# Optimization experiments

Measured on AMD Instinct MI355X. Metric: run time of the kernel, lower is better.

## Reference

```python
import jax, jax.numpy as jnp
import numpy as np
import math

B, L, DIM, H = 2, 2048, 512, 8


def setup_inputs() -> dict:
    key = jax.random.key(0)
    ks = jax.random.split(key, 8)
    s = 0.02
    return {
        "x": jax.random.normal(ks[0], (B, L, DIM), dtype=jnp.float32),
        "Wq": jax.random.normal(ks[1], (DIM, DIM), dtype=jnp.float32) * s,
        "Wk": jax.random.normal(ks[2], (DIM, DIM), dtype=jnp.float32) * s,
        "Wv": jax.random.normal(ks[3], (DIM, DIM), dtype=jnp.float32) * s,
        "Wb": jax.random.normal(ks[4], (H, DIM), dtype=jnp.float32) * s,   # content_bias weight
        "mixing": jax.random.normal(ks[5], (H, DIM), dtype=jnp.float32) * 0.2,  # UNIFORM init, std=0.2
        "Wd": jax.random.normal(ks[6], (DIM, DIM), dtype=jnp.float32) * s,
        "bd": jax.random.normal(ks[7], (DIM,), dtype=jnp.float32) * s,
    }


def reference(x, Wq, Wk, Wv, Wb, mixing, Wd, bd):
    b, l, d = x.shape
    h = mixing.shape[0]
    dh = d // h
    q = x @ Wq.T                      # [B,L,D]
    k = x @ Wk.T                      # [B,S,D]
    v = (x @ Wv.T).reshape(b, l, h, dh).transpose(0, 2, 1, 3)  # [B,H,S,dh]
    # scores[b,h,l,s] = sum_d q[b,l,d] * mixing[h,d] * k[b,s,d]
    scores = jnp.einsum("bld,hd,bsd->bhls", q, mixing, k)
    # content bias: [B,S,H] -> broadcast over query positions as [B,H,1,S]
    cb = jnp.einsum("bsd,hd->bhs", x, Wb)
    scale = math.sqrt(d / h)  # attention_head_size = dim / num_heads
    scores = (scores + cb[:, :, None, :]) / scale
    probs = jax.nn.softmax(scores, axis=-1)   # dropout disabled (eval)
    ctx = jnp.einsum("bhls,bhsd->bhld", probs, v)  # [B,H,L,dh]
    ctx = ctx.transpose(0, 2, 1, 3).reshape(b, l, d)
    return ctx @ Wd.T + bd
```

## Files before the change

### kernel.cpp

```cpp
#include <hip/hip_runtime.h>

#define B_ 2
#define L_ 2048
#define D_ 512
#define H_ 8
#define S_ 2048

typedef __attribute__((ext_vector_type(8))) short short8;
typedef __attribute__((ext_vector_type(8))) unsigned short ushort8;
typedef __attribute__((ext_vector_type(4))) unsigned short ushort4v;
typedef __attribute__((ext_vector_type(4))) float f32x4;
typedef __attribute__((ext_vector_type(16))) float f32x16;
typedef __attribute__((ext_vector_type(4))) float float4v;

__device__ __forceinline__ unsigned short f2bf(float f) {
    unsigned u = __float_as_uint(f);
    u += 0x7FFF + ((u >> 16) & 1);
    return (unsigned short)(u >> 16);
}
__device__ __forceinline__ float bf2f(unsigned short s) {
    return __uint_as_float(((unsigned)s) << 16);
}
__device__ __forceinline__ unsigned char f2fp8(float f) {
    return (unsigned char)(__builtin_amdgcn_cvt_pk_fp8_f32(f, f, 0, false) & 0xff);
}
__device__ __forceinline__ long pack8fp8(const float* v) {
    int lo = __builtin_amdgcn_cvt_pk_fp8_f32(v[0], v[1], 0, false);
    lo = __builtin_amdgcn_cvt_pk_fp8_f32(v[2], v[3], lo, true);
    int hi = __builtin_amdgcn_cvt_pk_fp8_f32(v[4], v[5], 0, false);
    hi = __builtin_amdgcn_cvt_pk_fp8_f32(v[6], v[7], hi, true);
    union { int i[2]; long l; } u;
    u.i[0] = lo; u.i[1] = hi;
    return u.l;
}
__device__ __forceinline__ int swap23(int x) {
    return (x & ~12) | ((x & 4) << 1) | ((x & 8) >> 1);
}
__device__ __forceinline__ void async16(void* lds, const void* g) {
    __builtin_amdgcn_global_load_lds(
        (const __attribute__((address_space(1))) void*)(g),
        (__attribute__((address_space(3))) void*)(lds), 16, 0, 0);
}

__global__ __launch_bounds__(256) void cvt_cb(const float* __restrict__ x,
                                              const float* __restrict__ w0, const float* __restrict__ w1,
                                              const float* __restrict__ w2, const float* __restrict__ w3,
                                              const float* __restrict__ Wb,
                                              unsigned short* __restrict__ xb,
                                              unsigned short* __restrict__ d0, unsigned short* __restrict__ d1,
                                              unsigned short* __restrict__ d2, unsigned short* __restrict__ d3,
                                              float* __restrict__ cbf) {
    if (blockIdx.x < 3072) {
        int i = blockIdx.x * 256 + threadIdx.x;
        const float* s;
        unsigned short* d;
        int idx;
        if (i < 524288) { s = x; d = xb; idx = i; }
        else {
            int off = i - 524288;
            int wsel = off >> 16; idx = off & 65535;
            s = (wsel == 0) ? w0 : (wsel == 1) ? w1 : (wsel == 2) ? w2 : w3;
            d = (wsel == 0) ? d0 : (wsel == 1) ? d1 : (wsel == 2) ? d2 : d3;
        }
        float4v v = *(const float4v*)(s + (size_t)idx * 4);
        ushort4v o;
        o[0] = f2bf(v[0]); o[1] = f2bf(v[1]); o[2] = f2bf(v[2]); o[3] = f2bf(v[3]);
        *(ushort4v*)(d + (size_t)idx * 4) = o;
    } else {
        const int tid = threadIdx.x, w = tid >> 6, lane = tid & 63;
        const int row = (blockIdx.x - 3072) * 4 + w;
        const int h = lane >> 3, seg = lane & 7;
        const float* xp = x + (size_t)row * 512 + seg * 64;
        const float* wp = Wb + (size_t)h * 512 + seg * 64;
        float acc = 0.f;
        #pragma unroll
        for (int j = 0; j < 16; ++j) {
            float4v xv = *(const float4v*)(xp + j * 4);
            float4v wv = *(const float4v*)(wp + j * 4);
            acc += xv[0] * wv[0] + xv[1] * wv[1] + xv[2] * wv[2] + xv[3] * wv[3];
        }
        acc += __shfl_xor(acc, 1);
        acc += __shfl_xor(acc, 2);
        acc += __shfl_xor(acc, 4);
        if (seg == 0) {
            int b = row >> 11, s = row & 2047;
            int T = s >> 5, off = s & 31;
            int r2 = off & 3, k = off >> 2;
            int u = (k & 1) + ((k >> 2) << 1), hi2 = (k >> 1) & 1;
            int R = 4 * u + r2;
            cbf[((size_t)((b * 8 + h) * 64 + T)) * 32 + hi2 * 16 + R] = acc * 0.125f * 1.44269504f;
        }
    }
}

__device__ __forceinline__ void gemm128_core(const unsigned short* __restrict__ Ap,
                                             const unsigned short* __restrict__ Bp,
                                             short* sA, short* sB, int tid, f32x4 c[4][4]) {
    const int w = tid >> 6, lane = tid & 63, quad = lane >> 4, l15 = lane & 15;
    const int wm = (w >> 1) * 64, wn = (w & 1) * 64;
    for (int kc = 0; kc < 8; ++kc) {
        __syncthreads();
        #pragma unroll
        for (int j = 0; j < 4; ++j) {
            int i = tid + j * 256;
            int row = i >> 3, seg = i & 7;
            *(ushort8*)&sA[row * 72 + seg * 8] = *(const ushort8*)(Ap + (size_t)row * 512 + kc * 64 + seg * 8);
            *(ushort8*)&sB[row * 72 + seg * 8] = *(const ushort8*)(Bp + (size_t)row * 512 + kc * 64 + seg * 8);
        }
        __syncthreads();
        #pragma unroll
        for (int ks = 0; ks < 2; ++ks) {
            short8 a[4], b[4];
            #pragma unroll
            for (int ii = 0; ii < 4; ++ii)
                a[ii] = *(const short8*)&sA[(wm + ii * 16 + l15) * 72 + ks * 32 + quad * 8];
            #pragma unroll
            for (int jj = 0; jj < 4; ++jj)
                b[jj] = *(const short8*)&sB[(wn + jj * 16 + l15) * 72 + ks * 32 + quad * 8];
            #pragma unroll
            for (int ii = 0; ii < 4; ++ii)
                #pragma unroll
                for (int jj = 0; jj < 4; ++jj)
                    c[ii][jj] = __builtin_amdgcn_mfma_f32_16x16x32_bf16(a[ii], b[jj], c[ii][jj], 0, 0, 0);
        }
    }
}

__global__ __launch_bounds__(256) void gemm_qkv(const unsigned short* __restrict__ xb,
                                                const unsigned short* __restrict__ Wqb,
                                                const unsigned short* __restrict__ Wkb,
                                                const unsigned short* __restrict__ Wvb,
                                                unsigned short* __restrict__ qb,
                                                unsigned char* __restrict__ kpack8,
                                                unsigned short* __restrict__ vfrag) {
    __shared__ short sA[128 * 72];
    __shared__ short sB[128 * 72];
    const int m0 = blockIdx.x * 128, n0 = blockIdx.y * 128, z = blockIdx.z;
    const unsigned short* Bsel = (z == 0) ? Wqb : ((z == 1) ? Wkb : Wvb);
    f32x4 c[4][4];
    #pragma unroll
    for (int ii = 0; ii < 4; ++ii)
        #pragma unroll
        for (int jj = 0; jj < 4; ++jj) { f32x4 zv = {0.f, 0.f, 0.f, 0.f}; c[ii][jj] = zv; }
    gemm128_core(xb + (size_t)m0 * 512, Bsel + (size_t)n0 * 512, sA, sB, threadIdx.x, c);
    const int tid = threadIdx.x, w = tid >> 6, lane = tid & 63, quad = lane >> 4, l15 = lane & 15;
    const int wm = (w >> 1) * 64, wn = (w & 1) * 64;
    #pragma unroll
    for (int ii = 0; ii < 4; ++ii) {
        const int mb = m0 + wm + ii * 16 + quad * 4;
        const int bb = mb >> 11;
        if (z == 0) {
            #pragma unroll
            for (int jj = 0; jj < 4; ++jj) {
                int ncol = n0 + wn + jj * 16 + l15;
                #pragma unroll
                for (int r = 0; r < 4; ++r)
                    qb[(size_t)(mb + r) * 512 + ncol] = f2bf(c[ii][jj][r]);
            }
        } else if (z == 1) {
            #pragma unroll
            for (int jj = 0; jj < 4; ++jj) {
                int d = n0 + wn + jj * 16 + l15;
                int pair = d >> 5, fh = (d >> 4) & 1, hid = (d >> 3) & 1, jq = d & 7;
                #pragma unroll
                for (int r = 0; r < 4; ++r) {
                    int s = (mb + r) & 2047;
                    int t = s >> 5, rr = swap23(s & 31);
                    kpack8[(((size_t)(bb * 64 + t) * 16 + pair) << 10)
                           + (hid * 32 + rr) * 16 + fh * 8 + jq] = f2fp8(c[ii][jj][r] * 32.f);
                }
            }
        } else {
            const int hh = (n0 + wn) >> 6;
            const int s = mb & 2047;
            #pragma unroll
            for (int jj = 0; jj < 4; ++jj) {
                int dh = jj * 16 + l15;
                ushort4v o;
                o[0] = f2bf(c[ii][jj][0]); o[1] = f2bf(c[ii][jj][1]);
                o[2] = f2bf(c[ii][jj][2]); o[3] = f2bf(c[ii][jj][3]);
                size_t blk = ((size_t)(bb * H_ + hh) * 64 + (s >> 5)) * 4
                           + ((dh >> 5) * 2 + ((s >> 4) & 1));
                *(ushort4v*)(vfrag + blk * 512 + (dh & 31) * 8 + ((s >> 3) & 1) * 256 + (s & 7)) = o;
            }
        }
    }
}

__global__ __launch_bounds__(256) void gemm_out(const unsigned short* __restrict__ ctxb,
                                                const unsigned short* __restrict__ Wdb,
                                                const float* __restrict__ bd,
                                                float* __restrict__ out) {
    __shared__ short sA[128 * 72];
    __shared__ short sB[128 * 72];
    const int m0 = blockIdx.x * 128, n0 = blockIdx.y * 128;
    f32x4 c[4][4];
    #pragma unroll
    for (int ii = 0; ii < 4; ++ii)
        #pragma unroll
        for (int jj = 0; jj < 4; ++jj) { f32x4 zv = {0.f, 0.f, 0.f, 0.f}; c[ii][jj] = zv; }
    gemm128_core(ctxb + (size_t)m0 * 512, Wdb + (size_t)n0 * 512, sA, sB, threadIdx.x, c);
    const int tid = threadIdx.x, w = tid >> 6, lane = tid & 63, quad = lane >> 4, l15 = lane & 15;
    const int wm = (w >> 1) * 64, wn = (w & 1) * 64;
    #pragma unroll
    for (int ii = 0; ii < 4; ++ii) {
        const int mb = m0 + wm + ii * 16 + quad * 4;
        #pragma unroll
        for (int jj = 0; jj < 4; ++jj) {
            int ncol = n0 + wn + jj * 16 + l15;
            float bias = bd[ncol];
            #pragma unroll
            for (int r = 0; r < 4; ++r)
                out[(size_t)(mb + r) * 512 + ncol] = c[ii][jj][r] + bias;
        }
    }
}

__global__ __launch_bounds__(256, 2) void flash_attn(const unsigned short* __restrict__ qb,
                                                     const unsigned char* __restrict__ kpack8,
                                                     const unsigned short* __restrict__ vfrag,
                                                     const float* __restrict__ cbf_all,
                                                     const float* __restrict__ mixing,
                                                     _Float16* __restrict__ Opart,
                                                     float* __restrict__ lpart) {
    __shared__ char sK[4][8192];
    const int bid = blockIdx.x;
    const int half = bid & 1, b = (bid >> 1) & 1, h = (bid >> 2) & 7, qt = bid >> 5;
    const int tid = threadIdx.x, w = tid >> 6, lane = tid & 63;
    const int l31 = lane & 31, hi = lane >> 5;
    const int q0 = qt * 128 + w * 32;
    const unsigned short* vfb = vfrag + ((size_t)(b * H_ + h) * 64 + half * 32) * 2048;
    const float* cbfb = cbf_all + ((size_t)((b * 8 + h) * 64 + half * 32)) * 32 + hi * 16;
    const float* mixh = mixing + h * D_;
    const float SC = 1.44269504f / 4096.0f;

    long qq[32];
    {
        const unsigned short* qrow = qb + ((size_t)(b * L_) + q0 + l31) * D_ + hi * 8;
        #pragma unroll
        for (int i = 0; i < 32; ++i) {
            ushort8 qv = *(const ushort8*)(qrow + i * 16);
            float4v ma = *(const float4v*)(mixh + i * 16 + hi * 8);
            float4v mb = *(const float4v*)(mixh + i * 16 + hi * 8 + 4);
            float v[8];
            v[0] = bf2f(qv[0]) * ma[0] * 16.f;
            v[1] = bf2f(qv[1]) * ma[1] * 16.f;
            v[2] = bf2f(qv[2]) * ma[2] * 16.f;
            v[3] = bf2f(qv[3]) * ma[3] * 16.f;
            v[4] = bf2f(qv[4]) * mb[0] * 16.f;
            v[5] = bf2f(qv[5]) * mb[1] * 16.f;
            v[6] = bf2f(qv[6]) * mb[2] * 16.f;
            v[7] = bf2f(qv[7]) * mb[3] * 16.f;
            qq[i] = pack8fp8(v);
        }
    }
    asm volatile("s_waitcnt vmcnt(0)" ::: "memory");

    f32x16 acco0, acco1;
    #pragma unroll
    for (int i = 0; i < 16; ++i) { acco0[i] = 0.f; acco1[i] = 0.f; }
    float lsum = 0.f;
    f32x16 aA0, aB0, aA1, aB1;
    short8 av00, av01, av10, av11;
    float4v cbf0, cbf1, cbf2, cbf3;

    auto stageK = [&](int p) {
        const char* src = (const char*)kpack8 + (((size_t)(b * 64 + half * 32)) << 14) + (size_t)p * 8192;
        char* dst = &sK[p & 3][0];
        #pragma unroll
        for (int ii = 0; ii < 2; ++ii)
            async16(dst + w * 1024 + ii * 4096, src + w * 1024 + ii * 4096 + (size_t)lane * 16);
    };
    auto ldV = [&](int t) {
        const unsigned short* vp = vfb + (size_t)t * 2048 + lane * 8;
        av00 = *(const short8*)(vp);
        av01 = *(const short8*)(vp + 512);
        av10 = *(const short8*)(vp + 1024);
        av11 = *(const short8*)(vp + 1536);
        asm volatile("" ::: "memory");
    };
    auto ldCB = [&](int t) {
        const float* cp = cbfb + t * 32;
        cbf0 = *(const float4v*)(cp);
        cbf1 = *(const float4v*)(cp + 4);
        cbf2 = *(const float4v*)(cp + 8);
        cbf3 = *(const float4v*)(cp + 12);
        asm volatile("" ::: "memory");
    };
    auto cbfv = [&](int R) -> float {
        return (R < 4) ? cbf0[R & 3] : (R < 8) ? cbf1[R & 3] : (R < 12) ? cbf2[R & 3] : cbf3[R & 3];
    };
    auto qk_chunk = [&](const char* buf, int qbase, f32x16& A, f32x16& B) {
        __builtin_amdgcn_s_setprio(1);
        #pragma unroll
        for (int p = 0; p < 8; ++p) {
            const long* ap = (const long*)&buf[p * 1024 + lane * 16];
            long a0 = ap[0], a1 = ap[1];
            A = __builtin_amdgcn_mfma_f32_32x32x16_fp8_fp8(a0, qq[qbase + 2 * p], A, 0, 0, 0);
            B = __builtin_amdgcn_mfma_f32_32x32x16_fp8_fp8(a1, qq[qbase + 2 * p + 1], B, 0, 0, 0);
        }
        __builtin_amdgcn_s_setprio(0);
    };
    auto pack_pv = [&](const float* pex) {
        union { unsigned int u[4]; short8 s8; } P0, P1;
        #pragma unroll
        for (int j = 0; j < 4; ++j) {
            P0.u[j] = __builtin_amdgcn_perm(__float_as_uint(pex[2 * j + 1]) + 0x8000u,
                                            __float_as_uint(pex[2 * j]) + 0x8000u, 0x07060302u);
            P1.u[j] = __builtin_amdgcn_perm(__float_as_uint(pex[8 + 2 * j + 1]) + 0x8000u,
                                            __float_as_uint(pex[8 + 2 * j]) + 0x8000u, 0x07060302u);
        }
        acco0 = __builtin_amdgcn_mfma_f32_32x32x16_bf16(av00, P0.s8, acco0, 0, 0, 0);
        acco0 = __builtin_amdgcn_mfma_f32_32x32x16_bf16(av01, P1.s8, acco0, 0, 0, 0);
        acco1 = __builtin_amdgcn_mfma_f32_32x32x16_bf16(av10, P0.s8, acco1, 0, 0, 0);
        acco1 = __builtin_amdgcn_mfma_f32_32x32x16_bf16(av11, P1.s8, acco1, 0, 0, 0);
    };
    auto qk_sm = [&](const char* buf, f32x16& CA, f32x16& CB, const f32x16& PA, const f32x16& PB) {
        __builtin_amdgcn_s_setprio(1);
        float pex[16];
        float lsA = 0.f, lsB = 0.f;
        #pragma unroll
        for (int p = 0; p < 8; ++p) {
            const long* ap = (const long*)&buf[p * 1024 + lane * 16];
            long a0 = ap[0], a1 = ap[1];
            CA = __builtin_amdgcn_mfma_f32_32x32x16_fp8_fp8(a0, qq[2 * p], CA, 0, 0, 0);
            CB = __builtin_amdgcn_mfma_f32_32x32x16_fp8_fp8(a1, qq[2 * p + 1], CB, 0, 0, 0);
            float x0 = fmaf(PA[2 * p] + PB[2 * p], SC, cbfv(2 * p));
            float x1 = fmaf(PA[2 * p + 1] + PB[2 * p + 1], SC, cbfv(2 * p + 1));
            float e0, e1;
            asm("v_exp_f32 %0, %1" : "=v"(e0) : "v"(x0));
            asm("v_exp_f32 %0, %1" : "=v"(e1) : "v"(x1));
            pex[2 * p] = e0; pex[2 * p + 1] = e1;
            lsA += e0; lsB += e1;
        }
        lsum += lsA + lsB;
        pack_pv(pex);
        __builtin_amdgcn_s_setprio(0);
    };
    auto sm_pv = [&](const f32x16& PA, const f32x16& PB) {
        float pex[16];
        float lsA = 0.f, lsB = 0.f;
        #pragma unroll
        for (int R = 0; R < 16; R += 2) {
            float x0 = fmaf(PA[R] + PB[R], SC, cbfv(R));
            float x1 = fmaf(PA[R + 1] + PB[R + 1], SC, cbfv(R + 1));
            float e0, e1;
            asm("v_exp_f32 %0, %1" : "=v"(e0) : "v"(x0));
            asm("v_exp_f32 %0, %1" : "=v"(e1) : "v"(x1));
            pex[R] = e0; pex[R + 1] = e1;
            lsA += e0; lsB += e1;
        }
        lsum += lsA + lsB;
        pack_pv(pex);
    };
    auto zero16 = [](f32x16& v) {
        #pragma unroll
        for (int i = 0; i < 16; ++i) v[i] = 0.f;
    };

    stageK(0); stageK(1); stageK(2);

    zero16(aA0); zero16(aB0);
    asm volatile("s_waitcnt vmcnt(4)" ::: "memory");
    __builtin_amdgcn_s_barrier();
    stageK(3);
    qk_chunk(&sK[0][0], 0, aA0, aB0);
    ldV(0); ldCB(0);
    asm volatile("s_waitcnt vmcnt(12)" ::: "memory");
    __builtin_amdgcn_s_barrier();
    stageK(4);
    qk_chunk(&sK[1][0], 16, aA0, aB0);

    #define E_TILE(T, CA, CB, PA, PB, BK)                                          \
        zero16(CA); zero16(CB);                                                    \
        asm volatile("s_waitcnt vmcnt(2)" ::: "memory");                           \
        __builtin_amdgcn_s_barrier();                                              \
        stageK(2 * (T) + 3);                                                       \
        qk_sm(&sK[BK][0], CA, CB, PA, PB);                                         \
        ldV(T); ldCB(T);
    #define O_TILE(T, CA, CB, BK)                                                  \
        __builtin_amdgcn_s_barrier();                                              \
        if ((T) < 30) stageK(2 * (T) + 4);                                         \
        qk_chunk(&sK[BK][0], 16, CA, CB);

    for (int tt = 1; tt < 30; tt += 2) {
        E_TILE(tt, aA1, aB1, aA0, aB0, 2);
        O_TILE(tt, aA1, aB1, 3);
        E_TILE(tt + 1, aA0, aB0, aA1, aB1, 0);
        O_TILE(tt + 1, aA0, aB0, 1);
    }
    #undef E_TILE
    #undef O_TILE

    {
        zero16(aA1); zero16(aB1);
        asm volatile("s_waitcnt vmcnt(0)" ::: "memory");
        __builtin_amdgcn_s_barrier();
        qk_sm(&sK[2][0], aA1, aB1, aA0, aB0);
        ldV(31); ldCB(31);
        __builtin_amdgcn_s_barrier();
        qk_chunk(&sK[3][0], 16, aA1, aB1);
        asm volatile("s_waitcnt vmcnt(0)" ::: "memory");
        sm_pv(aA1, aB1);
    }

    lsum += __shfl_xor(lsum, 32);
    if (hi == 0) lpart[(size_t)bid * 128 + w * 32 + l31] = lsum;
    #pragma unroll
    for (int R = 0; R < 16; ++R) {
        int dh = (R & 3) + 8 * (R >> 2) + 4 * hi;
        Opart[((size_t)bid * 64 + dh) * 128 + w * 32 + l31] = (_Float16)acco0[R];
        Opart[((size_t)bid * 64 + 32 + dh) * 128 + w * 32 + l31] = (_Float16)acco1[R];
    }
}

__global__ __launch_bounds__(256) void merge_ctx(const _Float16* __restrict__ Opart,
                                                 const float* __restrict__ lpart,
                                                 unsigned short* __restrict__ ctxb) {
    int t = blockIdx.x * 256 + threadIdx.x;
    int qq = t & 127, dh4 = (t >> 7) & 15, qt = (t >> 11) & 15, h = (t >> 15) & 7, b = t >> 18;
    int base = (qt << 5) | (h << 2) | (b << 1);
    float l = lpart[(size_t)base * 128 + qq] + lpart[(size_t)(base + 1) * 128 + qq];
    float inv = 1.f / l;
    ushort4v o;
    #pragma unroll
    for (int e = 0; e < 4; ++e) {
        int dh = dh4 * 4 + e;
        float v = (float)Opart[((size_t)base * 64 + dh) * 128 + qq]
                + (float)Opart[((size_t)(base + 1) * 64 + dh) * 128 + qq];
        o[e] = f2bf(v * inv);
    }
    *(ushort4v*)(ctxb + ((size_t)(b * L_) + qt * 128 + qq) * 512 + h * 64 + dh4 * 4) = o;
}

extern "C" void kernel_launch(void* const* d_in, const int* in_sizes, int n_in,
                              void* d_out, int out_size, void* d_ws, size_t ws_size,
                              hipStream_t stream) {
    (void)in_sizes; (void)n_in; (void)out_size; (void)ws_size;
    const float* x      = (const float*)d_in[0];
    const float* Wq     = (const float*)d_in[1];
    const float* Wk     = (const float*)d_in[2];
    const float* Wv     = (const float*)d_in[3];
    const float* Wb     = (const float*)d_in[4];
    const float* mixing = (const float*)d_in[5];
    const float* Wd     = (const float*)d_in[6];
    const float* bd     = (const float*)d_in[7];
    float* out = (float*)d_out;

    char* ws = (char*)d_ws;
    const size_t MiB = 1048576;
    unsigned short* xb     = (unsigned short*)(ws);
    unsigned short* qb     = (unsigned short*)(ws + 4 * MiB);
    unsigned char*  kpack8 = (unsigned char*)(ws + 8 * MiB);
    unsigned short* vfrag  = (unsigned short*)(ws + 10 * MiB);
    unsigned short* ctxb   = (unsigned short*)(ws + 14 * MiB);
    unsigned short* Wqb    = (unsigned short*)(ws + 18 * MiB);
    unsigned short* Wkb    = (unsigned short*)(ws + 18 * MiB + 512 * 1024);
    unsigned short* Wvb    = (unsigned short*)(ws + 19 * MiB);
    unsigned short* Wdb    = (unsigned short*)(ws + 19 * MiB + 512 * 1024);
    float* cbuf            = (float*)(ws + 20 * MiB);
    float* lpart           = (float*)(ws + 20 * MiB + 256 * 1024);
    _Float16* Opart        = (_Float16*)(ws + 21 * MiB);

    cvt_cb<<<4096, 256, 0, stream>>>(x, Wq, Wk, Wv, Wd, Wb, xb, Wqb, Wkb, Wvb, Wdb, cbuf);
    gemm_qkv<<<dim3(32, 4, 3), 256, 0, stream>>>(xb, Wqb, Wkb, Wvb, qb, kpack8, vfrag);
    flash_attn<<<512, 256, 0, stream>>>(qb, kpack8, vfrag, cbuf, mixing, Opart, lpart);
    merge_ctx<<<2048, 256, 0, stream>>>(Opart, lpart, ctxb);
    gemm_out<<<dim3(32, 4), 256, 0, stream>>>(ctxb, Wdb, bd, out);
}
```

Baseline: 201.9 us.

## Restage K as full tiles in a triple buffer with one barrier per tile

The K staging pipeline moves from four half-tile LDS buffers, with a barrier every half tile, to three full-tile buffers, with one barrier and one waitcnt per 128-key tile. QK MFMAs for a whole tile now run in one fused loop. The exp/pack/PV work for the previous tile and the V and content-bias loads for the current one are spread across that loop. The aim is to halve synchronisation points and overlap global loads with MFMA work. The cost is more LDS per block (48KB), which could limit how many blocks fit per CU.

```diff
diff --git a/kernel.cpp b/kernel.cpp
--- a/kernel.cpp
+++ b/kernel.cpp
@@ -223,7 +223,7 @@
                                                      const float* __restrict__ mixing,
                                                      _Float16* __restrict__ Opart,
                                                      float* __restrict__ lpart) {
-    __shared__ char sK[4][8192];
+    __shared__ char sK[3][16384];
     const int bid = blockIdx.x;
     const int half = bid & 1, b = (bid >> 1) & 1, h = (bid >> 2) & 7, qt = bid >> 5;
     const int tid = threadIdx.x, w = tid >> 6, lane = tid & 63;
@@ -264,11 +264,11 @@
     short8 av00, av01, av10, av11;
     float4v cbf0, cbf1, cbf2, cbf3;
 
-    auto stageK = [&](int p) {
-        const char* src = (const char*)kpack8 + (((size_t)(b * 64 + half * 32)) << 14) + (size_t)p * 8192;
-        char* dst = &sK[p & 3][0];
-        #pragma unroll
-        for (int ii = 0; ii < 2; ++ii)
+    auto stageK2 = [&](int t, int bi) {
+        const char* src = (const char*)kpack8 + (((size_t)(b * 64 + half * 32 + t)) << 14);
+        char* dst = &sK[bi][0];
+        #pragma unroll
+        for (int ii = 0; ii < 4; ++ii)
             async16(dst + w * 1024 + ii * 4096, src + w * 1024 + ii * 4096 + (size_t)lane * 16);
     };
     auto ldV = [&](int t) {
@@ -290,17 +290,6 @@
     auto cbfv = [&](int R) -> float {
         return (R < 4) ? cbf0[R & 3] : (R < 8) ? cbf1[R & 3] : (R < 12) ? cbf2[R & 3] : cbf3[R & 3];
     };
-    auto qk_chunk = [&](const char* buf, int qbase, f32x16& A, f32x16& B) {
-        __builtin_amdgcn_s_setprio(1);
-        #pragma unroll
-        for (int p = 0; p < 8; ++p) {
-            const long* ap = (const long*)&buf[p * 1024 + lane * 16];
-            long a0 = ap[0], a1 = ap[1];
-            A = __builtin_amdgcn_mfma_f32_32x32x16_fp8_fp8(a0, qq[qbase + 2 * p], A, 0, 0, 0);
-            B = __builtin_amdgcn_mfma_f32_32x32x16_fp8_fp8(a1, qq[qbase + 2 * p + 1], B, 0, 0, 0);
-        }
-        __builtin_amdgcn_s_setprio(0);
-    };
     auto pack_pv = [&](const float* pex) {
         union { unsigned int u[4]; short8 s8; } P0, P1;
         #pragma unroll
@@ -315,26 +304,43 @@
         acco1 = __builtin_amdgcn_mfma_f32_32x32x16_bf16(av10, P0.s8, acco1, 0, 0, 0);
         acco1 = __builtin_amdgcn_mfma_f32_32x32x16_bf16(av11, P1.s8, acco1, 0, 0, 0);
     };
-    auto qk_sm = [&](const char* buf, f32x16& CA, f32x16& CB, const f32x16& PA, const f32x16& PB) {
+    auto tile_fused = [&](const char* buf, int T, f32x16& CA, f32x16& CB,
+                          const f32x16& PA, const f32x16& PB) {
         __builtin_amdgcn_s_setprio(1);
         float pex[16];
         float lsA = 0.f, lsB = 0.f;
         #pragma unroll
-        for (int p = 0; p < 8; ++p) {
-            const long* ap = (const long*)&buf[p * 1024 + lane * 16];
+        for (int fp = 0; fp < 16; ++fp) {
+            const long* ap = (const long*)&buf[fp * 1024 + lane * 16];
             long a0 = ap[0], a1 = ap[1];
-            CA = __builtin_amdgcn_mfma_f32_32x32x16_fp8_fp8(a0, qq[2 * p], CA, 0, 0, 0);
-            CB = __builtin_amdgcn_mfma_f32_32x32x16_fp8_fp8(a1, qq[2 * p + 1], CB, 0, 0, 0);
-            float x0 = fmaf(PA[2 * p] + PB[2 * p], SC, cbfv(2 * p));
-            float x1 = fmaf(PA[2 * p + 1] + PB[2 * p + 1], SC, cbfv(2 * p + 1));
-            float e0, e1;
-            asm("v_exp_f32 %0, %1" : "=v"(e0) : "v"(x0));
-            asm("v_exp_f32 %0, %1" : "=v"(e1) : "v"(x1));
-            pex[2 * p] = e0; pex[2 * p + 1] = e1;
-            lsA += e0; lsB += e1;
-        }
-        lsum += lsA + lsB;
-        pack_pv(pex);
+            CA = __builtin_amdgcn_mfma_f32_32x32x16_fp8_fp8(a0, qq[2 * fp], CA, 0, 0, 0);
+            CB = __builtin_amdgcn_mfma_f32_32x32x16_fp8_fp8(a1, qq[2 * fp + 1], CB, 0, 0, 0);
+            if (fp < 8) {
+                float x0 = fmaf(PA[2 * fp] + PB[2 * fp], SC, cbfv(2 * fp));
+                float x1 = fmaf(PA[2 * fp + 1] + PB[2 * fp + 1], SC, cbfv(2 * fp + 1));
+                float e0, e1;
+                asm("v_exp_f32 %0, %1" : "=v"(e0) : "v"(x0));
+                asm("v_exp_f32 %0, %1" : "=v"(e1) : "v"(x1));
+                pex[2 * fp] = e0; pex[2 * fp + 1] = e1;
+                lsA += e0; lsB += e1;
+            }
+            if (fp == 8) { lsum += lsA + lsB; pack_pv(pex); }
+            if (fp == 9)  ldV(T);
+            if (fp == 10) ldCB(T);
+        }
+        __builtin_amdgcn_s_setprio(0);
+    };
+    auto tile_plain = [&](const char* buf, int T, f32x16& CA, f32x16& CB) {
+        __builtin_amdgcn_s_setprio(1);
+        #pragma unroll
+        for (int fp = 0; fp < 16; ++fp) {
+            const long* ap = (const long*)&buf[fp * 1024 + lane * 16];
+            long a0 = ap[0], a1 = ap[1];
+            CA = __builtin_amdgcn_mfma_f32_32x32x16_fp8_fp8(a0, qq[2 * fp], CA, 0, 0, 0);
+            CB = __builtin_amdgcn_mfma_f32_32x32x16_fp8_fp8(a1, qq[2 * fp + 1], CB, 0, 0, 0);
+            if (fp == 9)  ldV(T);
+            if (fp == 10) ldCB(T);
+        }
         __builtin_amdgcn_s_setprio(0);
     };
     auto sm_pv = [&](const f32x16& PA, const f32x16& PB) {
@@ -358,48 +364,36 @@
         for (int i = 0; i < 16; ++i) v[i] = 0.f;
     };
 
-    stageK(0); stageK(1); stageK(2);
+    stageK2(0, 0); stageK2(1, 1);
 
     zero16(aA0); zero16(aB0);
     asm volatile("s_waitcnt vmcnt(4)" ::: "memory");
     __builtin_amdgcn_s_barrier();
-    stageK(3);
-    qk_chunk(&sK[0][0], 0, aA0, aB0);
-    ldV(0); ldCB(0);
-    asm volatile("s_waitcnt vmcnt(12)" ::: "memory");
-    __builtin_amdgcn_s_barrier();
-    stageK(4);
-    qk_chunk(&sK[1][0], 16, aA0, aB0);
-
-    #define E_TILE(T, CA, CB, PA, PB, BK)                                          \
-        zero16(CA); zero16(CB);                                                    \
-        asm volatile("s_waitcnt vmcnt(2)" ::: "memory");                           \
-        __builtin_amdgcn_s_barrier();                                              \
-        stageK(2 * (T) + 3);                                                       \
-        qk_sm(&sK[BK][0], CA, CB, PA, PB);                                         \
-        ldV(T); ldCB(T);
-    #define O_TILE(T, CA, CB, BK)                                                  \
-        __builtin_amdgcn_s_barrier();                                              \
-        if ((T) < 30) stageK(2 * (T) + 4);                                         \
-        qk_chunk(&sK[BK][0], 16, CA, CB);
-
-    for (int tt = 1; tt < 30; tt += 2) {
-        E_TILE(tt, aA1, aB1, aA0, aB0, 2);
-        O_TILE(tt, aA1, aB1, 3);
-        E_TILE(tt + 1, aA0, aB0, aA1, aB1, 0);
-        O_TILE(tt + 1, aA0, aB0, 1);
-    }
-    #undef E_TILE
-    #undef O_TILE
+    tile_plain(&sK[0][0], 0, aA0, aB0);
+    stageK2(2, 2);
+
+    int cur = 1;
+    for (int t = 1; t <= 30; t += 2) {
+        zero16(aA1); zero16(aB1);
+        asm volatile("s_waitcnt vmcnt(4)" ::: "memory");
+        __builtin_amdgcn_s_barrier();
+        tile_fused(&sK[cur][0], t, aA1, aB1, aA0, aB0);
+        if (t + 2 <= 31) stageK2(t + 2, (cur + 2 >= 3) ? cur - 1 : cur + 2);
+        cur = (cur == 2) ? 0 : cur + 1;
+
+        zero16(aA0); zero16(aB0);
+        asm volatile("s_waitcnt vmcnt(4)" ::: "memory");
+        __builtin_amdgcn_s_barrier();
+        tile_fused(&sK[cur][0], t + 1, aA0, aB0, aA1, aB1);
+        if (t + 3 <= 31) stageK2(t + 3, (cur + 2 >= 3) ? cur - 1 : cur + 2);
+        cur = (cur == 2) ? 0 : cur + 1;
+    }
 
     {
         zero16(aA1); zero16(aB1);
         asm volatile("s_waitcnt vmcnt(0)" ::: "memory");
         __builtin_amdgcn_s_barrier();
-        qk_sm(&sK[2][0], aA1, aB1, aA0, aB0);
-        ldV(31); ldCB(31);
-        __builtin_amdgcn_s_barrier();
-        qk_chunk(&sK[3][0], 16, aA1, aB1);
+        tile_fused(&sK[cur][0], 31, aA1, aB1, aA0, aB0);
         asm volatile("s_waitcnt vmcnt(0)" ::: "memory");
         sm_pv(aA1, aB1);
     }
```

Result: no change. 198.3 us (-1.8%).
